# Kernel optimization log

Measured on AMD Instinct MI355X. Metric: run time of the kernel, lower is better.

## Reference

```python
import jax, jax.numpy as jnp
import numpy as np

N_POINTS = 65536      # total nodes across the batch
NDIMS = 3
NUM_THETAS = 64       # directions
BUMP_STEPS = 32       # discretization steps of [-radius, radius]
NUM_GRAPHS = 64       # number of point clouds in the batch
RADIUS = 1.1
SCALE = 100.0         # sigmoid sharpness


def setup_inputs() -> dict:
    key = jax.random.key(0)
    k1, k2, k3 = jax.random.split(key, 3)
    x = jax.random.normal(k1, (N_POINTS, NDIMS), dtype=jnp.float32)
    # unit-norm direction vectors on the sphere, columns of v: [ndims, num_thetas]
    v = jax.random.normal(k2, (NDIMS, NUM_THETAS), dtype=jnp.float32)
    v = v / jnp.linalg.norm(v, axis=0, keepdims=True)
    # lin = discretization of [-radius, radius], matches nn.Parameter linspace
    lin = jnp.linspace(-RADIUS, RADIUS, BUMP_STEPS, dtype=jnp.float32)
    # sorted batch index assigning each node to a graph (torch_geometric convention)
    batch = jnp.sort(jax.random.randint(k3, (N_POINTS,), 0, NUM_GRAPHS, dtype=jnp.int32))
    return {"x": x, "v": v, "lin": lin, "batch": batch}


def reference(x, v, lin, batch):
    # node heights: inner product of coordinates with each direction -> [N, T]
    nh = x @ v
    # broadcast soft-threshold: sigmoid(scale * (lin - nh)) -> [N, S, T]
    # (torch builds [S,1,N,T] then movedims to [N,1,S,T]; same values)
    ecc = jax.nn.sigmoid(SCALE * (lin[None, :, None] - nh[:, None, :]))
    # segment scatter-add over nodes per graph -> [B, S, T]
    ect = jax.ops.segment_sum(ecc, batch, num_segments=NUM_GRAPHS)
    return ect  # torch output after .squeeze(): [batch, bump_steps, num_thetas]
```

## Files before the change

### kernel.cpp

```cpp
#include <hip/hip_runtime.h>

#define T      64
#define S      32
#define NGRAPH 64
#define NSPLIT 16
#define NW     4

__global__ __launch_bounds__(256, 4) void ect_partial(
    const float* __restrict__ x, const float* __restrict__ v,
    const float* __restrict__ lin, const int* __restrict__ batch,
    float* __restrict__ ws, int n_points)
{
    __shared__ float bins[256 * 33];
    __shared__ float v0s[256];

    const int tid  = threadIdx.x;
    const int t    = tid & 63;
    const int w    = tid >> 6;
    const int b    = blockIdx.x;
    const int g    = b >> 4;
    const int c    = b & (NSPLIT - 1);

    for (int i = tid; i < 256 * 33; i += 256) bins[i] = 0.0f;

    const int target = (t < 32) ? g : (g + 1);
    const int i32    = t & 31;
    int lo = 0;
    const int strides[3] = {2048, 64, 2};
#pragma unroll
    for (int rnd = 0; rnd < 3; rnd++) {
        const int stride = strides[rnd];
        const int idx  = lo + i32 * stride;
        const int pv   = batch[min(idx, n_points - 1)];
        const bool prd = (idx < n_points) && (pv < target);
        const unsigned long long bal = __ballot(prd);
        const int cnt = __popc((unsigned)(bal >> (t & 32)));
        lo += max(cnt - 1, 0) * stride;
    }
#pragma unroll
    for (int rnd = 0; rnd < 2; rnd++) {
        const int idx = min(lo, n_points - 1);
        if ((lo < n_points) && (batch[idx] < target)) lo++;
    }
    const int gstart = __shfl(lo, 0);
    const int gend   = __shfl(lo, 32);
    const int len    = gend - gstart;
    const int n0     = gstart + (len * c) / NSPLIT;
    const int n1     = gstart + (len * (c + 1)) / NSPLIT;

    const float lin0     = lin[0];
    const float step     = lin[1] - lin0;
    const float inv_step = 1.0f / step;
    const float K2 = (100.0f * step) * 1.4426950408889634f;
    const float r  = __builtin_amdgcn_exp2f(-K2);

    const float v0 = v[0 * T + t];
    const float v1 = v[1 * T + t];
    const float v2 = v[2 * T + t];

    float v0acc = 0.0f;
    const int binb = tid * 33;

#pragma unroll 2
    for (int n = n0 + w; n < n1; n += NW) {
        const float* xp = x + 3 * n;
        const float nh = fmaf(xp[0], v0, fmaf(xp[1], v1, xp[2] * v2));
        const float f  = (nh - lin0) * inv_step;
        const float fs = ceilf(f);
        const int   ss = (int)fs;
        const float gg = fs - f;
        const float e0 = __builtin_amdgcn_exp2f(fmaf(-K2, gg, K2));
        const float e1 = e0 * r;
        const float e2 = e1 * r;
        const float sm  = __builtin_amdgcn_rcpf(1.0f + e0);
        const float s0v = __builtin_amdgcn_rcpf(1.0f + e1);
        const float sp  = __builtin_amdgcn_rcpf(1.0f + e2);
        v0acc += (ss >= 2) ? 0.0f
               : (ss == 1) ? sm
               : (ss == 0) ? s0v
               : (ss == -1) ? sp : 1.0f;
        const int p0 = ss - 1, p1 = ss, p2 = ss + 1, p3 = ss + 2;
        const int a0 = binb + (((unsigned)(p0 - 1) < 31u) ? p0 : 0);
        const int a1 = binb + (((unsigned)(p1 - 1) < 31u) ? p1 : 0);
        const int a2 = binb + (((unsigned)(p2 - 1) < 31u) ? p2 : 0);
        const int a3 = binb + (((unsigned)(p3 - 1) < 31u) ? p3 : 0);
        const float r0 = bins[a0], r1 = bins[a1], r2 = bins[a2], r3 = bins[a3];
        bins[a0] = r0 + sm;
        bins[a1] = r1 + (s0v - sm);
        bins[a2] = r2 + (sp - s0v);
        bins[a3] = r3 + (1.0f - sp);
    }

    v0s[tid] = v0acc;
    __syncthreads();

    for (int cell = tid; cell < 64 * 33; cell += 256) {
        const int tt = cell & 63;
        const int cc = cell >> 6;
        const float sum = bins[(0 * 64 + tt) * 33 + cc] + bins[(1 * 64 + tt) * 33 + cc]
                        + bins[(2 * 64 + tt) * 33 + cc] + bins[(3 * 64 + tt) * 33 + cc];
        bins[tt * 33 + cc] = sum;
    }
    if (tid < 64) v0s[tid] += v0s[64 + tid] + v0s[128 + tid] + v0s[192 + tid];
    __syncthreads();

    float run = v0s[t];
    const int sbase = 8 * w;
    for (int cc = 1; cc < sbase; cc++) run += bins[t * 33 + cc];
    float* wsb = ws + (size_t)b * (S * T);
#pragma unroll
    for (int j = 0; j < 8; j++) {
        const int s = sbase + j;
        if (s >= 1) run += bins[t * 33 + s];
        wsb[s * T + t] = run;
    }
}

__global__ __launch_bounds__(256) void ect_reduce(
    const float* __restrict__ ws, float* __restrict__ out)
{
    const int idx = blockIdx.x * 256 + threadIdx.x;
    const int g   = idx >> 11;
    const int i   = idx & 2047;
    float sum = 0.0f;
#pragma unroll
    for (int c = 0; c < NSPLIT; c++)
        sum += ws[(size_t)(g * NSPLIT + c) * (S * T) + i];
    out[idx] = sum;
}

extern "C" void kernel_launch(void* const* d_in, const int* in_sizes, int n_in,
                              void* d_out, int out_size, void* d_ws, size_t ws_size,
                              hipStream_t stream) {
    const float* x     = (const float*)d_in[0];
    const float* v     = (const float*)d_in[1];
    const float* lin   = (const float*)d_in[2];
    const int*   batch = (const int*)d_in[3];
    float* out = (float*)d_out;
    float* ws  = (float*)d_ws;

    const int n_points = in_sizes[0] / 3;

    ect_partial<<<NGRAPH * NSPLIT, 256, 0, stream>>>(x, v, lin, batch, ws, n_points);
    ect_reduce<<<NGRAPH * S * T / 256, 256, 0, stream>>>(ws, out);
}
```

Before: 76.52 us.

## Use three-bin sigmoid difference updates and move prefix scan into reduce kernel

The per-point scatter drops from four LDS read-modify-writes and three sigmoids to three of each. This assumes the third neighbouring sigmoid is already saturated at this scale and step, so it is folded into 1. The partial kernel now writes unscanned 33-column histograms straight to the workspace and skips its second sync. The cumulative prefix scan over steps moves into a reduce kernel with one block per graph, which accumulates the splits in registers and then scans through LDS. The bins padding changes to 34 with a dummy slot 33 for out-of-range hits, and the shuffles become readlane. The dropped sigmoid term adds a small approximation error, and the reduce kernel now launches only 64 blocks.

```diff
diff --git a/kernel.cpp b/kernel.cpp
--- a/kernel.cpp
+++ b/kernel.cpp
@@ -11,8 +11,7 @@
     const float* __restrict__ lin, const int* __restrict__ batch,
     float* __restrict__ ws, int n_points)
 {
-    __shared__ float bins[256 * 33];
-    __shared__ float v0s[256];
+    __shared__ float bins[256 * 34];
 
     const int tid  = threadIdx.x;
     const int t    = tid & 63;
@@ -21,7 +20,7 @@
     const int g    = b >> 4;
     const int c    = b & (NSPLIT - 1);
 
-    for (int i = tid; i < 256 * 33; i += 256) bins[i] = 0.0f;
+    for (int i = tid; i < 256 * 34; i += 256) bins[i] = 0.0f;
 
     const int target = (t < 32) ? g : (g + 1);
     const int i32    = t & 31;
@@ -42,8 +41,8 @@
         const int idx = min(lo, n_points - 1);
         if ((lo < n_points) && (batch[idx] < target)) lo++;
     }
-    const int gstart = __shfl(lo, 0);
-    const int gend   = __shfl(lo, 32);
+    const int gstart = __builtin_amdgcn_readfirstlane(lo);
+    const int gend   = __builtin_amdgcn_readlane(lo, 32);
     const int len    = gend - gstart;
     const int n0     = gstart + (len * c) / NSPLIT;
     const int n1     = gstart + (len * (c + 1)) / NSPLIT;
@@ -51,6 +50,7 @@
     const float lin0     = lin[0];
     const float step     = lin[1] - lin0;
     const float inv_step = 1.0f / step;
+    const float nl0i     = -lin0 * inv_step;
     const float K2 = (100.0f * step) * 1.4426950408889634f;
     const float r  = __builtin_amdgcn_exp2f(-K2);
 
@@ -59,74 +59,81 @@
     const float v2 = v[2 * T + t];
 
     float v0acc = 0.0f;
-    const int binb = tid * 33;
+    const int binb = tid * 34;
 
 #pragma unroll 2
     for (int n = n0 + w; n < n1; n += NW) {
-        const float* xp = x + 3 * n;
-        const float nh = fmaf(xp[0], v0, fmaf(xp[1], v1, xp[2] * v2));
-        const float f  = (nh - lin0) * inv_step;
+        const float x0 = x[3 * n + 0];
+        const float x1 = x[3 * n + 1];
+        const float x2 = x[3 * n + 2];
+        const float nh = fmaf(x0, v0, fmaf(x1, v1, x2 * v2));
+        const float f  = fmaf(nh, inv_step, nl0i);
         const float fs = ceilf(f);
         const int   ss = (int)fs;
-        const float gg = fs - f;
-        const float e0 = __builtin_amdgcn_exp2f(fmaf(-K2, gg, K2));
+        const float e0 = __builtin_amdgcn_exp2f(fmaf(K2, f - fs, K2));
         const float e1 = e0 * r;
-        const float e2 = e1 * r;
         const float sm  = __builtin_amdgcn_rcpf(1.0f + e0);
         const float s0v = __builtin_amdgcn_rcpf(1.0f + e1);
-        const float sp  = __builtin_amdgcn_rcpf(1.0f + e2);
-        v0acc += (ss >= 2) ? 0.0f
-               : (ss == 1) ? sm
-               : (ss == 0) ? s0v
-               : (ss == -1) ? sp : 1.0f;
-        const int p0 = ss - 1, p1 = ss, p2 = ss + 1, p3 = ss + 2;
-        const int a0 = binb + (((unsigned)(p0 - 1) < 31u) ? p0 : 0);
-        const int a1 = binb + (((unsigned)(p1 - 1) < 31u) ? p1 : 0);
-        const int a2 = binb + (((unsigned)(p2 - 1) < 31u) ? p2 : 0);
-        const int a3 = binb + (((unsigned)(p3 - 1) < 31u) ? p3 : 0);
-        const float r0 = bins[a0], r1 = bins[a1], r2 = bins[a2], r3 = bins[a3];
-        bins[a0] = r0 + sm;
-        bins[a1] = r1 + (s0v - sm);
-        bins[a2] = r2 + (sp - s0v);
-        bins[a3] = r3 + (1.0f - sp);
+        v0acc += (ss <= -1) ? 1.0f : (ss == 0 ? s0v : (ss == 1 ? sm : 0.0f));
+        const int p0 = ss - 1, p1 = ss, p2 = ss + 1;
+        const int a0 = binb + (((unsigned)(p0 - 1) < 31u) ? p0 : 33);
+        const int a1 = binb + (((unsigned)(p1 - 1) < 31u) ? p1 : 33);
+        const int a2 = binb + (((unsigned)(p2 - 1) < 31u) ? p2 : 33);
+        bins[a0] += sm;
+        bins[a1] += s0v - sm;
+        bins[a2] += 1.0f - s0v;
     }
 
-    v0s[tid] = v0acc;
+    bins[binb + 0] = v0acc;
     __syncthreads();
 
-    for (int cell = tid; cell < 64 * 33; cell += 256) {
+    float* wsb = ws + (size_t)b * (33 * 64);
+    for (int cell = tid; cell < 33 * 64; cell += 256) {
+        const int cc = cell >> 6;
         const int tt = cell & 63;
-        const int cc = cell >> 6;
-        const float sum = bins[(0 * 64 + tt) * 33 + cc] + bins[(1 * 64 + tt) * 33 + cc]
-                        + bins[(2 * 64 + tt) * 33 + cc] + bins[(3 * 64 + tt) * 33 + cc];
-        bins[tt * 33 + cc] = sum;
-    }
-    if (tid < 64) v0s[tid] += v0s[64 + tid] + v0s[128 + tid] + v0s[192 + tid];
-    __syncthreads();
-
-    float run = v0s[t];
-    const int sbase = 8 * w;
-    for (int cc = 1; cc < sbase; cc++) run += bins[t * 33 + cc];
-    float* wsb = ws + (size_t)b * (S * T);
-#pragma unroll
-    for (int j = 0; j < 8; j++) {
-        const int s = sbase + j;
-        if (s >= 1) run += bins[t * 33 + s];
-        wsb[s * T + t] = run;
+        const float sum = bins[(  0 + tt) * 34 + cc] + bins[( 64 + tt) * 34 + cc]
+                        + bins[(128 + tt) * 34 + cc] + bins[(192 + tt) * 34 + cc];
+        wsb[cell] = sum;
     }
 }
 
 __global__ __launch_bounds__(256) void ect_reduce(
     const float* __restrict__ ws, float* __restrict__ out)
 {
-    const int idx = blockIdx.x * 256 + threadIdx.x;
-    const int g   = idx >> 11;
-    const int i   = idx & 2047;
-    float sum = 0.0f;
+    __shared__ float red[33 * 64];
+    const int g   = blockIdx.x;
+    const int tid = threadIdx.x;
+
+    float a[9];
 #pragma unroll
-    for (int c = 0; c < NSPLIT; c++)
-        sum += ws[(size_t)(g * NSPLIT + c) * (S * T) + i];
-    out[idx] = sum;
+    for (int k = 0; k < 9; k++) a[k] = 0.0f;
+#pragma unroll 1
+    for (int i = 0; i < NSPLIT; i++) {
+        const float* wsb = ws + (size_t)(g * NSPLIT + i) * (33 * 64);
+#pragma unroll
+        for (int k = 0; k < 9; k++) {
+            const int cell = tid + 256 * k;
+            if (cell < 33 * 64) a[k] += wsb[cell];
+        }
+    }
+#pragma unroll
+    for (int k = 0; k < 9; k++) {
+        const int cell = tid + 256 * k;
+        if (cell < 33 * 64) red[cell] = a[k];
+    }
+    __syncthreads();
+
+    const int t = tid & 63;
+    const int w = tid >> 6;
+    float run = red[t];
+    for (int cc = 1; cc < 8 * w; cc++) run += red[cc * 64 + t];
+    float* og = out + g * (S * T);
+#pragma unroll
+    for (int j = 0; j < 8; j++) {
+        const int s = 8 * w + j;
+        if (s >= 1) run += red[s * 64 + t];
+        og[s * 64 + t] = run;
+    }
 }
 
 extern "C" void kernel_launch(void* const* d_in, const int* in_sizes, int n_in,
@@ -142,5 +149,5 @@
     const int n_points = in_sizes[0] / 3;
 
     ect_partial<<<NGRAPH * NSPLIT, 256, 0, stream>>>(x, v, lin, batch, ws, n_points);
-    ect_reduce<<<NGRAPH * S * T / 256, 256, 0, stream>>>(ws, out);
+    ect_reduce<<<NGRAPH, 256, 0, stream>>>(ws, out);
 }
```

Measured after the change: 94.20 us. 1.23x slower.
